# Kernel tuning notes

Measured on AMD Instinct MI355X. Metric: run time of the kernel, lower is better.

Reference implementation:

```python
import math
import jax, jax.numpy as jnp
import numpy as np

QDEPTH = 8
WIDTH = 32
HEIGHT = 32
PIXELS = WIDTH * HEIGHT          # 1024
WIRES = int(math.ceil(math.log2(PIXELS)))  # 10, and PIXELS == 2**WIRES exactly
BATCH = 2048


def setup_inputs() -> dict:
    key = jax.random.key(0)
    k1, k2 = jax.random.split(key)
    x = jax.random.normal(k1, (BATCH, 1, WIDTH, HEIGHT), dtype=jnp.float32)
    # torch.randn(weight_shape) * 0.4
    weights = jax.random.normal(k2, (QDEPTH, WIRES, 3), dtype=jnp.float32) * 0.4
    return {"x": x, "weights": weights, "reps": 1}


def _apply_1q(s, U, wire):
    # s: (batch, 2, 2, ..., 2); apply 2x2 unitary U on qubit `wire` (axis wire+1)
    ax = wire + 1
    s = jnp.moveaxis(s, ax, -1)
    s = s @ U.T                      # new[..., i] = sum_j U[i, j] * old[..., j]
    return jnp.moveaxis(s, -1, ax)


def _apply_cnot(s, ctrl, tgt):
    # flip target bit on the control==1 half of the state
    c_ax = ctrl + 1
    t_ax = tgt + 1
    s0 = jnp.take(s, 0, axis=c_ax)
    s1 = jnp.take(s, 1, axis=c_ax)
    t = t_ax - 1 if t_ax > c_ax else t_ax
    s1 = jnp.flip(s1, axis=t)
    return jnp.stack([s0, s1], axis=c_ax)


def _rot_matrix(phi, theta, omega):
    # qml.Rot = RZ(phi) -> RY(theta) -> RZ(omega)
    c = jnp.cos(theta * 0.5)
    sn = jnp.sin(theta * 0.5)
    ep = jnp.exp(-0.5j * (phi + omega))   # e^{-i(phi+omega)/2}
    em = jnp.exp(-0.5j * (phi - omega))   # e^{-i(phi-omega)/2}
    return jnp.stack([
        jnp.stack([ep * c, -jnp.conj(em) * sn]),
        jnp.stack([em * sn, jnp.conj(ep) * c]),
    ]).astype(jnp.complex64)


def _circuit(psi, weights, reps):
    # psi: (batch, 2**WIRES) complex64 normalized state
    b = psi.shape[0]
    s = psi.reshape((b,) + (2,) * WIRES)
    w = jnp.tanh(weights)                 # qw_map.tanh
    # StronglyEntanglingLayers default ranges: r_l = l % (wires-1) + 1
    ranges = [(l % (WIRES - 1)) + 1 for l in range(QDEPTH)]
    for _ in range(reps):
        for l in range(QDEPTH):
            for q in range(WIRES):
                U = _rot_matrix(w[l, q, 0], w[l, q, 1], w[l, q, 2])
                s = _apply_1q(s, U, q)
            r = ranges[l]
            for q in range(WIRES):
                s = _apply_cnot(s, q, (q + r) % WIRES)
    return s.reshape(b, 2 ** WIRES)


def reference(x, weights, reps):
    b = x.shape[0]
    v = x.reshape(b, PIXELS)                       # b 1 w h -> b (w h)
    old_norm = jnp.linalg.norm(v, axis=-1, keepdims=True)
    psi = (v / old_norm).astype(jnp.complex64)     # real amplitudes, zero imag
    out = _circuit(psi, weights, reps)
    out = out * old_norm.astype(jnp.complex64)
    return out.reshape(b, 1, WIDTH, HEIGHT)
```

## Files before the change

### kernel.cpp

```cpp
#include <hip/hip_runtime.h>
#include <math.h>


#define WIRES   10
#define NSTATE  1024
#define QDEPTH  8
#define NBATCH  2048
#define NGATES  (QDEPTH * WIRES)

typedef float v2f __attribute__((ext_vector_type(2)));
typedef unsigned int v2u __attribute__((ext_vector_type(2)));
static __device__ __forceinline__ v2f s2(float x) { return (v2f){x, x}; }

#define WS_WORDS 1280

__device__ __forceinline__ int perm_g(int j, int r) {
#pragma unroll
    for (int q = WIRES - 1; q >= 0; --q) {
        const int cb = 9 - q;
        const int tb = 9 - ((q + r) % WIRES);
        j ^= ((j >> cb) & 1) << tb;
    }
    return j;
}

__global__ __launch_bounds__(1024) void qprep(
    const float* __restrict__ weights, float* __restrict__ ws)
{
    const int tid = threadIdx.x;
    if (tid < NGATES) {
        const float phi   = tanhf(weights[tid * 3 + 0]);
        const float theta = tanhf(weights[tid * 3 + 1]);
        const float omega = tanhf(weights[tid * 3 + 2]);
        const float c  = cosf(theta * 0.5f);
        const float sn = sinf(theta * 0.5f);
        const float a  = 0.5f * (phi + omega);
        const float bb = 0.5f * (phi - omega);
        const float ca = cosf(a),  sa = sinf(a);
        const float cb = cosf(bb), sb = sinf(bb);
        ws[tid * 8 + 0] =  ca * c;  ws[tid * 8 + 1] = -sa * c;
        ws[tid * 8 + 2] = -cb * sn; ws[tid * 8 + 3] = -sb * sn;
        ws[tid * 8 + 4] =  cb * sn; ws[tid * 8 + 5] = -sb * sn;
        ws[tid * 8 + 6] =  ca * c;  ws[tid * 8 + 7] =  sa * c;
    }
    int* wsI = (int*)ws;
    if (tid >= 128 && tid < 256) {
        const int e = tid - 128, l = e >> 4, t = e & 15;
        const int j = perm_g(t, (l % (WIRES - 1)) + 1);
        wsI[640 + e] = ((j & 15) << 6) | (j >> 4);
    }
    if (tid >= 256 && tid < 768) {
        const int e = tid - 256, l = e >> 6, v = e & 63;
        const int j = perm_g(v << 4, (l % (WIRES - 1)) + 1);
        wsI[768 + e] = ((j & 15) << 6) | (j >> 4);
    }
}

template<int CTRL>
__device__ __forceinline__ float dppmov(float x) {
    return __int_as_float(__builtin_amdgcn_update_dpp(
        0, __float_as_int(x), CTRL, 0xF, 0xF, true));
}
#define FX1(v)  dppmov<0xB1>(v)
#define FX2(v)  dppmov<0x4E>(v)
#define FX4(v)  dppmov<0x1B>(dppmov<0x141>(v))
#define FX8(v)  dppmov<0x128>(v)

#if __has_builtin(__builtin_amdgcn_permlane16_swap)
static __device__ __forceinline__ float pl16swap(float x) {
    const v2u r = __builtin_amdgcn_permlane16_swap(
        __float_as_uint(x), __float_as_uint(x), false, false);
    return __uint_as_float((threadIdx.x & 16) ? r.x : r.y);
}
#define FX16(v) pl16swap(v)
#else
#define FX16(v) __shfl_xor((v), 16, 64)
#endif

#if __has_builtin(__builtin_amdgcn_permlane32_swap)
static __device__ __forceinline__ float pl32swap(float x) {
    const v2u r = __builtin_amdgcn_permlane32_swap(
        __float_as_uint(x), __float_as_uint(x), false, false);
    return __uint_as_float((threadIdx.x & 32) ? r.x : r.y);
}
#define FX32(v) pl32swap(v)
#else
#define FX32(v) __shfl_xor((v), 32, 64)
#endif

#define APPLY_LOCAL_PK(uptr, mask)                                            \
    {                                                                         \
        const float* __restrict__ u = (uptr);                                 \
        const float u00r=u[0], u00i=u[1], u01r=u[2], u01i=u[3];               \
        const float u10r=u[4], u10i=u[5], u11r=u[6], u11i=u[7];               \
        _Pragma("unroll")                                                     \
        for (int k0 = 0; k0 < 8; ++k0) {                                      \
            if (k0 & (mask)) continue;                                        \
            const int k1 = k0 | (mask);                                       \
            const v2f a0r = zr[k0], a0i = zi[k0];                             \
            const v2f a1r = zr[k1], a1i = zi[k1];                             \
            zr[k0] = s2(u00r)*a0r - s2(u00i)*a0i + s2(u01r)*a1r - s2(u01i)*a1i;\
            zi[k0] = s2(u00r)*a0i + s2(u00i)*a0r + s2(u01r)*a1i + s2(u01i)*a1r;\
            zr[k1] = s2(u10r)*a0r - s2(u10i)*a0i + s2(u11r)*a1r - s2(u11i)*a1i;\
            zi[k1] = s2(u10r)*a0i + s2(u10i)*a0r + s2(u11r)*a1i + s2(u11i)*a1r;\
        }                                                                     \
    }

#define LANE_GATE_PK(W, J, FETCH)                                             \
    {                                                                         \
        const float* __restrict__ u = gw + (W) * 8;                           \
        const bool hi = (lane >> (J)) & 1;                                    \
        const float c0r = hi ? u[6] : u[0], c0i = hi ? u[7] : u[1];           \
        const float c1r = hi ? u[4] : u[2], c1i = hi ? u[5] : u[3];           \
        _Pragma("unroll")                                                     \
        for (int k = 0; k < 8; ++k) {                                         \
            v2f pr, pi;                                                       \
            pr.x = FETCH(zr[k].x); pr.y = FETCH(zr[k].y);                     \
            pi.x = FETCH(zi[k].x); pi.y = FETCH(zi[k].y);                     \
            const v2f sr = zr[k], si = zi[k];                                 \
            zr[k] = s2(c0r)*sr - s2(c0i)*si + s2(c1r)*pr - s2(c1i)*pi;        \
            zi[k] = s2(c0r)*si + s2(c0i)*sr + s2(c1r)*pi + s2(c1i)*pr;        \
        }                                                                     \
    }

__global__ __launch_bounds__(64) void qsim_wave(
    const float* __restrict__ x,
    const float* __restrict__ ws,
    float* __restrict__ out,
    const int interleaved)
{
    __shared__ float lds[2 * NSTATE];
    const int lane = threadIdx.x;
    const int b    = blockIdx.x;
    const int* __restrict__ wsI = (const int*)ws;

    v2f zr[8], zi[8];

    const float4* __restrict__ x4 =
        (const float4*)(x + ((size_t)b << 10) + (lane << 4));
    {
        const float4 v0 = x4[0], v1 = x4[1], v2 = x4[2], v3 = x4[3];
        zr[0].x=v0.x; zr[1].x=v0.y; zr[2].x=v0.z; zr[3].x=v0.w;
        zr[4].x=v1.x; zr[5].x=v1.y; zr[6].x=v1.z; zr[7].x=v1.w;
        zr[0].y=v2.x; zr[1].y=v2.y; zr[2].y=v2.z; zr[3].y=v2.w;
        zr[4].y=v3.x; zr[5].y=v3.y; zr[6].y=v3.z; zr[7].y=v3.w;
#pragma unroll
        for (int k = 0; k < 8; ++k) zi[k] = (v2f){0.f, 0.f};
    }

    for (int l = 0; l < QDEPTH; ++l) {
        const float* __restrict__ gw = ws + l * 80;

        APPLY_LOCAL_PK(gw + 9*8, 1)
        APPLY_LOCAL_PK(gw + 8*8, 2)
        APPLY_LOCAL_PK(gw + 7*8, 4)

        {
            const float* __restrict__ u = gw + 6*8;
            const v2f pAr = (v2f){u[0], u[6]};
            const v2f pAi = (v2f){u[1], u[7]};
            const v2f pBr = (v2f){u[2], u[4]};
            const v2f pBi = (v2f){u[3], u[5]};
#pragma unroll
            for (int k = 0; k < 8; ++k) {
                const v2f r  = zr[k], i = zi[k];
                const v2f rs = __builtin_shufflevector(r, r, 1, 0);
                const v2f is = __builtin_shufflevector(i, i, 1, 0);
                zr[k] = pAr*r - pAi*i + pBr*rs - pBi*is;
                zi[k] = pAr*i + pAi*r + pBr*is + pBi*rs;
            }
        }

        LANE_GATE_PK(5, 0, FX1)
        LANE_GATE_PK(4, 1, FX2)
        LANE_GATE_PK(3, 2, FX4)
        LANE_GATE_PK(2, 3, FX8)
        LANE_GATE_PK(1, 4, FX16)
        LANE_GATE_PK(0, 5, FX32)

#pragma unroll
        for (int k = 0; k < 8; ++k) {
            const int w = k * 64 + lane;
            lds[w]        = zr[k].x;
            lds[w + 512]  = zr[k].y;
            lds[w + 1024] = zi[k].x;
            lds[w + 1536] = zi[k].y;
        }
        const int ga = wsI[768 + l * 64 + lane];
#pragma unroll
        for (int k = 0; k < 8; ++k) {
            const int a0 = ga ^ wsI[640 + l * 16 + k];
            const int a1 = ga ^ wsI[640 + l * 16 + k + 8];
            zr[k].x = lds[a0]; zi[k].x = lds[a0 + 1024];
            zr[k].y = lds[a1]; zi[k].y = lds[a1 + 1024];
        }
    }

    if (interleaved) {
        float2* __restrict__ o2 = (float2*)out;
        const size_t base = ((size_t)b << 10) + (lane << 4);
#pragma unroll
        for (int k = 0; k < 8; ++k) {
            o2[base + k]     = make_float2(zr[k].x, zi[k].x);
            o2[base + k + 8] = make_float2(zr[k].y, zi[k].y);
        }
    } else {
        float4* __restrict__ o4 = (float4*)(out + ((size_t)b << 10) + (lane << 4));
        o4[0] = make_float4(zr[0].x, zr[1].x, zr[2].x, zr[3].x);
        o4[1] = make_float4(zr[4].x, zr[5].x, zr[6].x, zr[7].x);
        o4[2] = make_float4(zr[0].y, zr[1].y, zr[2].y, zr[3].y);
        o4[3] = make_float4(zr[4].y, zr[5].y, zr[6].y, zr[7].y);
    }
}

__global__ __launch_bounds__(256) void qcircuit_kernel(
    const float* __restrict__ x, const float* __restrict__ weights,
    float* __restrict__ out, const int interleaved)
{
    __shared__ float s_re[NSTATE];
    __shared__ float s_im[NSTATE];
    __shared__ float s_g[NGATES][8];
    const int tid = threadIdx.x;
    const int b   = blockIdx.x;
    if (tid < NGATES) {
        const float phi   = tanhf(weights[tid * 3 + 0]);
        const float theta = tanhf(weights[tid * 3 + 1]);
        const float omega = tanhf(weights[tid * 3 + 2]);
        const float c  = cosf(theta * 0.5f);
        const float sn = sinf(theta * 0.5f);
        const float a  = 0.5f * (phi + omega);
        const float bb = 0.5f * (phi - omega);
        const float ca = cosf(a),  sa = sinf(a);
        const float cb = cosf(bb), sb = sinf(bb);
        s_g[tid][0] =  ca * c;  s_g[tid][1] = -sa * c;
        s_g[tid][2] = -cb * sn; s_g[tid][3] = -sb * sn;
        s_g[tid][4] =  cb * sn; s_g[tid][5] = -sb * sn;
        s_g[tid][6] =  ca * c;  s_g[tid][7] =  sa * c;
    }
#pragma unroll
    for (int k = 0; k < 4; ++k) {
        const int i = tid + 256 * k;
        s_re[i] = x[b * NSTATE + i];
        s_im[i] = 0.0f;
    }
    __syncthreads();
    for (int l = 0; l < QDEPTH; ++l) {
        for (int q = 0; q < WIRES; ++q) {
            const int gi = l * WIRES + q;
            const float u00r = s_g[gi][0], u00i = s_g[gi][1];
            const float u01r = s_g[gi][2], u01i = s_g[gi][3];
            const float u10r = s_g[gi][4], u10i = s_g[gi][5];
            const float u11r = s_g[gi][6], u11i = s_g[gi][7];
            const int sh = 9 - q;
            const int m  = 1 << sh;
#pragma unroll
            for (int k = 0; k < 2; ++k) {
                const int p  = tid + 256 * k;
                const int i0 = ((p >> sh) << (sh + 1)) | (p & (m - 1));
                const int i1 = i0 | m;
                const float a0r = s_re[i0], a0i = s_im[i0];
                const float a1r = s_re[i1], a1i = s_im[i1];
                s_re[i0] = u00r*a0r - u00i*a0i + u01r*a1r - u01i*a1i;
                s_im[i0] = u00r*a0i + u00i*a0r + u01r*a1i + u01i*a1r;
                s_re[i1] = u10r*a0r - u10i*a0i + u11r*a1r - u11i*a1i;
                s_im[i1] = u10r*a0i + u10i*a0r + u11r*a1i + u11i*a1r;
            }
            __syncthreads();
        }
        const int r = (l % (WIRES - 1)) + 1;
        float vr[4], vi[4];
#pragma unroll
        for (int k = 0; k < 4; ++k) {
            const int i = tid + 256 * k;
            const int j = perm_g(i, r);
            vr[k] = s_re[j]; vi[k] = s_im[j];
        }
        __syncthreads();
#pragma unroll
        for (int k = 0; k < 4; ++k) {
            const int i = tid + 256 * k;
            s_re[i] = vr[k]; s_im[i] = vi[k];
        }
        __syncthreads();
    }
    if (interleaved) {
#pragma unroll
        for (int k = 0; k < 4; ++k) {
            const int i  = tid + 256 * k;
            const int fi = 2 * (b * NSTATE + i);
            out[fi + 0] = s_re[i];
            out[fi + 1] = s_im[i];
        }
    } else {
#pragma unroll
        for (int k = 0; k < 4; ++k) {
            const int i = tid + 256 * k;
            out[b * NSTATE + i] = s_re[i];
        }
    }
}

extern "C" void kernel_launch(void* const* d_in, const int* in_sizes, int n_in,
                              void* d_out, int out_size, void* d_ws, size_t ws_size,
                              hipStream_t stream) {
    const float* x       = (const float*)d_in[0];
    const float* weights = (const float*)d_in[1];
    float* out = (float*)d_out;
    const int interleaved = (out_size >= 2 * NBATCH * NSTATE) ? 1 : 0;

    if (ws_size >= WS_WORDS * sizeof(float)) {
        float* ws = (float*)d_ws;
        qprep<<<1, 1024, 0, stream>>>(weights, ws);
        qsim_wave<<<NBATCH, 64, 0, stream>>>(x, ws, out, interleaved);
    } else {
        qcircuit_kernel<<<NBATCH, 256, 0, stream>>>(x, weights, out, interleaved);
    }
}
```

Measured before the change: 104.4 us.

## Split each batch state across two wavefronts with LDS exchange for one qubit

Each batch element's 1024-amplitude state is now spread over two 64-lane wavefronts instead of one, so each thread holds 4 packed register pairs rather than 8. One qubit that used to be local to a thread now spans the two waves, and its gate is applied by exchanging amplitudes through a shared-memory buffer behind a barrier. The goal is shorter per-thread dependency chains, lower register pressure and more waves in flight. The cost is two block-level barriers per layer and extra LDS traffic.

```diff
diff --git a/kernel.cpp b/kernel.cpp
--- a/kernel.cpp
+++ b/kernel.cpp
@@ -88,15 +88,15 @@
 #define FX32(v) __shfl_xor((v), 32, 64)
 #endif
 
-#define APPLY_LOCAL_PK(uptr, mask)                                            \
+#define APPLY_LOCAL_PK4(uptr, mask)                                           \
     {                                                                         \
         const float* __restrict__ u = (uptr);                                 \
         const float u00r=u[0], u00i=u[1], u01r=u[2], u01i=u[3];               \
         const float u10r=u[4], u10i=u[5], u11r=u[6], u11i=u[7];               \
         _Pragma("unroll")                                                     \
-        for (int k0 = 0; k0 < 8; ++k0) {                                      \
+        for (int k0 = 0; k0 < 4; ++k0) {                                      \
             if (k0 & (mask)) continue;                                        \
-            const int k1 = k0 | (mask);                                       \
+            const int k1 = k0 | (mask);                                      \
             const v2f a0r = zr[k0], a0i = zi[k0];                             \
             const v2f a1r = zr[k1], a1i = zi[k1];                             \
             zr[k0] = s2(u00r)*a0r - s2(u00i)*a0i + s2(u01r)*a1r - s2(u01i)*a1i;\
@@ -106,14 +106,14 @@
         }                                                                     \
     }
 
-#define LANE_GATE_PK(W, J, FETCH)                                             \
+#define LANE_GATE_PK4(W, J, FETCH)                                            \
     {                                                                         \
         const float* __restrict__ u = gw + (W) * 8;                           \
         const bool hi = (lane >> (J)) & 1;                                    \
         const float c0r = hi ? u[6] : u[0], c0i = hi ? u[7] : u[1];           \
         const float c1r = hi ? u[4] : u[2], c1i = hi ? u[5] : u[3];           \
         _Pragma("unroll")                                                     \
-        for (int k = 0; k < 8; ++k) {                                         \
+        for (int k = 0; k < 4; ++k) {                                         \
             v2f pr, pi;                                                       \
             pr.x = FETCH(zr[k].x); pr.y = FETCH(zr[k].y);                     \
             pi.x = FETCH(zi[k].x); pi.y = FETCH(zi[k].y);                     \
@@ -123,46 +123,47 @@
         }                                                                     \
     }
 
-__global__ __launch_bounds__(64) void qsim_wave(
+__global__ __launch_bounds__(128) void qsim_wave2(
     const float* __restrict__ x,
     const float* __restrict__ ws,
     float* __restrict__ out,
     const int interleaved)
 {
     __shared__ float lds[2 * NSTATE];
-    const int lane = threadIdx.x;
+    __shared__ v2f exb[2 * 4 * 2 * 64];
+
+    const int tid  = threadIdx.x;
+    const int lane = tid & 63;
+    const int w    = tid >> 6;
     const int b    = blockIdx.x;
     const int* __restrict__ wsI = (const int*)ws;
 
-    v2f zr[8], zi[8];
+    v2f zr[4], zi[4];
 
     const float4* __restrict__ x4 =
-        (const float4*)(x + ((size_t)b << 10) + (lane << 4));
+        (const float4*)(x + ((size_t)b << 10) + (lane << 4) + (w << 3));
     {
-        const float4 v0 = x4[0], v1 = x4[1], v2 = x4[2], v3 = x4[3];
+        const float4 v0 = x4[0], v1 = x4[1];
         zr[0].x=v0.x; zr[1].x=v0.y; zr[2].x=v0.z; zr[3].x=v0.w;
-        zr[4].x=v1.x; zr[5].x=v1.y; zr[6].x=v1.z; zr[7].x=v1.w;
-        zr[0].y=v2.x; zr[1].y=v2.y; zr[2].y=v2.z; zr[3].y=v2.w;
-        zr[4].y=v3.x; zr[5].y=v3.y; zr[6].y=v3.z; zr[7].y=v3.w;
-#pragma unroll
-        for (int k = 0; k < 8; ++k) zi[k] = (v2f){0.f, 0.f};
+        zr[0].y=v1.x; zr[1].y=v1.y; zr[2].y=v1.z; zr[3].y=v1.w;
+#pragma unroll
+        for (int k = 0; k < 4; ++k) zi[k] = (v2f){0.f, 0.f};
     }
 
     for (int l = 0; l < QDEPTH; ++l) {
         const float* __restrict__ gw = ws + l * 80;
 
-        APPLY_LOCAL_PK(gw + 9*8, 1)
-        APPLY_LOCAL_PK(gw + 8*8, 2)
-        APPLY_LOCAL_PK(gw + 7*8, 4)
+        APPLY_LOCAL_PK4(gw + 9*8, 1)
+        APPLY_LOCAL_PK4(gw + 8*8, 2)
 
         {
-            const float* __restrict__ u = gw + 6*8;
+            const float* __restrict__ u = gw + 7*8;
             const v2f pAr = (v2f){u[0], u[6]};
             const v2f pAi = (v2f){u[1], u[7]};
             const v2f pBr = (v2f){u[2], u[4]};
             const v2f pBi = (v2f){u[3], u[5]};
 #pragma unroll
-            for (int k = 0; k < 8; ++k) {
+            for (int k = 0; k < 4; ++k) {
                 const v2f r  = zr[k], i = zi[k];
                 const v2f rs = __builtin_shufflevector(r, r, 1, 0);
                 const v2f is = __builtin_shufflevector(i, i, 1, 0);
@@ -171,26 +172,49 @@
             }
         }
 
-        LANE_GATE_PK(5, 0, FX1)
-        LANE_GATE_PK(4, 1, FX2)
-        LANE_GATE_PK(3, 2, FX4)
-        LANE_GATE_PK(2, 3, FX8)
-        LANE_GATE_PK(1, 4, FX16)
-        LANE_GATE_PK(0, 5, FX32)
-
-#pragma unroll
-        for (int k = 0; k < 8; ++k) {
-            const int w = k * 64 + lane;
-            lds[w]        = zr[k].x;
-            lds[w + 512]  = zr[k].y;
-            lds[w + 1024] = zi[k].x;
-            lds[w + 1536] = zi[k].y;
-        }
+        {
+            const int wb = w * 512 + lane;
+            exb[wb +   0] = zr[0]; exb[wb +  64] = zi[0];
+            exb[wb + 128] = zr[1]; exb[wb + 192] = zi[1];
+            exb[wb + 256] = zr[2]; exb[wb + 320] = zi[2];
+            exb[wb + 384] = zr[3]; exb[wb + 448] = zi[3];
+            __syncthreads();
+            const float* __restrict__ u = gw + 6*8;
+            const bool hi = (w != 0);
+            const float c0r = hi ? u[6] : u[0], c0i = hi ? u[7] : u[1];
+            const float c1r = hi ? u[4] : u[2], c1i = hi ? u[5] : u[3];
+            const int pb = (w ^ 1) * 512 + lane;
+#pragma unroll
+            for (int k = 0; k < 4; ++k) {
+                const v2f pr = exb[pb + k * 128];
+                const v2f pi = exb[pb + k * 128 + 64];
+                const v2f sr = zr[k], si = zi[k];
+                zr[k] = s2(c0r)*sr - s2(c0i)*si + s2(c1r)*pr - s2(c1i)*pi;
+                zi[k] = s2(c0r)*si + s2(c0i)*sr + s2(c1r)*pi + s2(c1i)*pr;
+            }
+        }
+
+        LANE_GATE_PK4(5, 0, FX1)
+        LANE_GATE_PK4(4, 1, FX2)
+        LANE_GATE_PK4(3, 2, FX4)
+        LANE_GATE_PK4(2, 3, FX8)
+        LANE_GATE_PK4(1, 4, FX16)
+        LANE_GATE_PK4(0, 5, FX32)
+
+#pragma unroll
+        for (int k = 0; k < 4; ++k) {
+            const int ww = (w * 8 + k) * 64 + lane;
+            lds[ww]        = zr[k].x;
+            lds[ww + 256]  = zr[k].y;
+            lds[ww + 1024] = zi[k].x;
+            lds[ww + 1280] = zi[k].y;
+        }
+        __syncthreads();
         const int ga = wsI[768 + l * 64 + lane];
 #pragma unroll
-        for (int k = 0; k < 8; ++k) {
-            const int a0 = ga ^ wsI[640 + l * 16 + k];
-            const int a1 = ga ^ wsI[640 + l * 16 + k + 8];
+        for (int k = 0; k < 4; ++k) {
+            const int a0 = ga ^ wsI[640 + l * 16 + w * 8 + k];
+            const int a1 = ga ^ wsI[640 + l * 16 + w * 8 + k + 4];
             zr[k].x = lds[a0]; zi[k].x = lds[a0 + 1024];
             zr[k].y = lds[a1]; zi[k].y = lds[a1 + 1024];
         }
@@ -198,18 +222,17 @@
 
     if (interleaved) {
         float2* __restrict__ o2 = (float2*)out;
-        const size_t base = ((size_t)b << 10) + (lane << 4);
-#pragma unroll
-        for (int k = 0; k < 8; ++k) {
+        const size_t base = ((size_t)b << 10) + (lane << 4) + (w << 3);
+#pragma unroll
+        for (int k = 0; k < 4; ++k) {
             o2[base + k]     = make_float2(zr[k].x, zi[k].x);
-            o2[base + k + 8] = make_float2(zr[k].y, zi[k].y);
+            o2[base + k + 4] = make_float2(zr[k].y, zi[k].y);
         }
     } else {
-        float4* __restrict__ o4 = (float4*)(out + ((size_t)b << 10) + (lane << 4));
+        float4* __restrict__ o4 =
+            (float4*)(out + ((size_t)b << 10) + (lane << 4) + (w << 3));
         o4[0] = make_float4(zr[0].x, zr[1].x, zr[2].x, zr[3].x);
-        o4[1] = make_float4(zr[4].x, zr[5].x, zr[6].x, zr[7].x);
-        o4[2] = make_float4(zr[0].y, zr[1].y, zr[2].y, zr[3].y);
-        o4[3] = make_float4(zr[4].y, zr[5].y, zr[6].y, zr[7].y);
+        o4[1] = make_float4(zr[0].y, zr[1].y, zr[2].y, zr[3].y);
     }
 }
 
@@ -311,7 +334,7 @@
     if (ws_size >= WS_WORDS * sizeof(float)) {
         float* ws = (float*)d_ws;
         qprep<<<1, 1024, 0, stream>>>(weights, ws);
-        qsim_wave<<<NBATCH, 64, 0, stream>>>(x, ws, out, interleaved);
+        qsim_wave2<<<NBATCH, 128, 0, stream>>>(x, ws, out, interleaved);
     } else {
         qcircuit_kernel<<<NBATCH, 256, 0, stream>>>(x, weights, out, interleaved);
     }
```

Result: slower. 109.2 us (+4.6%).

## Process two batch states per wavefront to interleave independent gate chains

Applied to the files above, without the earlier changes.

Each 64-lane block now simulates two batch samples at once, holding two register-resident states and interleaving their gate applications, lane shuffles and LDS CNOT permutations. The grid is halved to 1024 blocks and LDS per block doubles. The aim is more instruction-level parallelism to hide shuffle and LDS latency, and amortised gate-weight loads. The cost is doubled register pressure, which may lower occupancy, and fewer blocks to spread across the CUs.

```diff
diff --git a/kernel.cpp b/kernel.cpp
--- a/kernel.cpp
+++ b/kernel.cpp
@@ -88,7 +88,7 @@
 #define FX32(v) __shfl_xor((v), 32, 64)
 #endif
 
-#define APPLY_LOCAL_PK(uptr, mask)                                            \
+#define APPLY_LOCAL_PK(uptr, mask, zr, zi)                                    \
     {                                                                         \
         const float* __restrict__ u = (uptr);                                 \
         const float u00r=u[0], u00i=u[1], u01r=u[2], u01i=u[3];               \
@@ -106,7 +106,24 @@
         }                                                                     \
     }
 
-#define LANE_GATE_PK(W, J, FETCH)                                             \
+#define HALF_SWAP_PK(uptr, zr, zi)                                            \
+    {                                                                         \
+        const float* __restrict__ u = (uptr);                                 \
+        const v2f pAr = (v2f){u[0], u[6]};                  \
+        const v2f pAi = (v2f){u[1], u[7]};                  \
+        const v2f pBr = (v2f){u[2], u[4]};                  \
+        const v2f pBi = (v2f){u[3], u[5]};                  \
+        _Pragma("unroll")                                                     \
+        for (int k = 0; k < 8; ++k) {                                         \
+            const v2f r  = zr[k], i = zi[k];                                  \
+            const v2f rs = __builtin_shufflevector(r, r, 1, 0);               \
+            const v2f is = __builtin_shufflevector(i, i, 1, 0);               \
+            zr[k] = pAr*r - pAi*i + pBr*rs - pBi*is;                          \
+            zi[k] = pAr*i + pAi*r + pBr*is + pBi*rs;                          \
+        }                                                                     \
+    }
+
+#define LANE_GATE_PK(W, J, FETCH, zr, zi)                                     \
     {                                                                         \
         const float* __restrict__ u = gw + (W) * 8;                           \
         const bool hi = (lane >> (J)) & 1;                                    \
@@ -123,93 +140,113 @@
         }                                                                     \
     }
 
-__global__ __launch_bounds__(64) void qsim_wave(
+#define CNOT_WRITE(zr, zi, BASE)                                              \
+    _Pragma("unroll")                                                         \
+    for (int k = 0; k < 8; ++k) {                                             \
+        const int w = (BASE) + k * 64 + lane;                                 \
+        lds[w]        = zr[k].x;                                              \
+        lds[w + 512]  = zr[k].y;                                              \
+        lds[w + 1024] = zi[k].x;                                              \
+        lds[w + 1536] = zi[k].y;                                              \
+    }
+
+#define CNOT_READ(zr, zi, BASE)                                               \
+    _Pragma("unroll")                                                         \
+    for (int k = 0; k < 8; ++k) {                                             \
+        const int a0 = ga ^ wsI[640 + l * 16 + k];                            \
+        const int a1 = ga ^ wsI[640 + l * 16 + k + 8];                        \
+        zr[k].x = lds[(BASE) + a0]; zi[k].x = lds[(BASE) + a0 + 1024];        \
+        zr[k].y = lds[(BASE) + a1]; zi[k].y = lds[(BASE) + a1 + 1024];        \
+    }
+
+#define LOAD_STATE(x4, zr, zi)                                                \
+    {                                                                         \
+        const float4 v0 = (x4)[0], v1 = (x4)[1], v2 = (x4)[2], v3 = (x4)[3];  \
+        zr[0].x=v0.x; zr[1].x=v0.y; zr[2].x=v0.z; zr[3].x=v0.w;               \
+        zr[4].x=v1.x; zr[5].x=v1.y; zr[6].x=v1.z; zr[7].x=v1.w;               \
+        zr[0].y=v2.x; zr[1].y=v2.y; zr[2].y=v2.z; zr[3].y=v2.w;               \
+        zr[4].y=v3.x; zr[5].y=v3.y; zr[6].y=v3.z; zr[7].y=v3.w;               \
+        _Pragma("unroll")                                                     \
+        for (int k = 0; k < 8; ++k) zi[k] = (v2f){0.f, 0.f};                  \
+    }
+
+__global__ __launch_bounds__(64) void qsim_dual(
     const float* __restrict__ x,
     const float* __restrict__ ws,
     float* __restrict__ out,
     const int interleaved)
 {
-    __shared__ float lds[2 * NSTATE];
+    __shared__ float lds[4 * NSTATE];
     const int lane = threadIdx.x;
     const int b    = blockIdx.x;
     const int* __restrict__ wsI = (const int*)ws;
 
-    v2f zr[8], zi[8];
-
-    const float4* __restrict__ x4 =
-        (const float4*)(x + ((size_t)b << 10) + (lane << 4));
-    {
-        const float4 v0 = x4[0], v1 = x4[1], v2 = x4[2], v3 = x4[3];
-        zr[0].x=v0.x; zr[1].x=v0.y; zr[2].x=v0.z; zr[3].x=v0.w;
-        zr[4].x=v1.x; zr[5].x=v1.y; zr[6].x=v1.z; zr[7].x=v1.w;
-        zr[0].y=v2.x; zr[1].y=v2.y; zr[2].y=v2.z; zr[3].y=v2.w;
-        zr[4].y=v3.x; zr[5].y=v3.y; zr[6].y=v3.z; zr[7].y=v3.w;
-#pragma unroll
-        for (int k = 0; k < 8; ++k) zi[k] = (v2f){0.f, 0.f};
-    }
+    v2f zrA[8], ziA[8], zrB[8], ziB[8];
+
+    const float4* __restrict__ x4A =
+        (const float4*)(x + ((size_t)(2 * b) << 10) + (lane << 4));
+    const float4* __restrict__ x4B =
+        (const float4*)(x + ((size_t)(2 * b + 1) << 10) + (lane << 4));
+    LOAD_STATE(x4A, zrA, ziA)
+    LOAD_STATE(x4B, zrB, ziB)
 
     for (int l = 0; l < QDEPTH; ++l) {
         const float* __restrict__ gw = ws + l * 80;
 
-        APPLY_LOCAL_PK(gw + 9*8, 1)
-        APPLY_LOCAL_PK(gw + 8*8, 2)
-        APPLY_LOCAL_PK(gw + 7*8, 4)
-
-        {
-            const float* __restrict__ u = gw + 6*8;
-            const v2f pAr = (v2f){u[0], u[6]};
-            const v2f pAi = (v2f){u[1], u[7]};
-            const v2f pBr = (v2f){u[2], u[4]};
-            const v2f pBi = (v2f){u[3], u[5]};
-#pragma unroll
-            for (int k = 0; k < 8; ++k) {
-                const v2f r  = zr[k], i = zi[k];
-                const v2f rs = __builtin_shufflevector(r, r, 1, 0);
-                const v2f is = __builtin_shufflevector(i, i, 1, 0);
-                zr[k] = pAr*r - pAi*i + pBr*rs - pBi*is;
-                zi[k] = pAr*i + pAi*r + pBr*is + pBi*rs;
-            }
-        }
-
-        LANE_GATE_PK(5, 0, FX1)
-        LANE_GATE_PK(4, 1, FX2)
-        LANE_GATE_PK(3, 2, FX4)
-        LANE_GATE_PK(2, 3, FX8)
-        LANE_GATE_PK(1, 4, FX16)
-        LANE_GATE_PK(0, 5, FX32)
-
-#pragma unroll
-        for (int k = 0; k < 8; ++k) {
-            const int w = k * 64 + lane;
-            lds[w]        = zr[k].x;
-            lds[w + 512]  = zr[k].y;
-            lds[w + 1024] = zi[k].x;
-            lds[w + 1536] = zi[k].y;
-        }
+        APPLY_LOCAL_PK(gw + 9*8, 1, zrA, ziA)
+        APPLY_LOCAL_PK(gw + 9*8, 1, zrB, ziB)
+        APPLY_LOCAL_PK(gw + 8*8, 2, zrA, ziA)
+        APPLY_LOCAL_PK(gw + 8*8, 2, zrB, ziB)
+        APPLY_LOCAL_PK(gw + 7*8, 4, zrA, ziA)
+        APPLY_LOCAL_PK(gw + 7*8, 4, zrB, ziB)
+
+        HALF_SWAP_PK(gw + 6*8, zrA, ziA)
+        HALF_SWAP_PK(gw + 6*8, zrB, ziB)
+
+        LANE_GATE_PK(5, 0, FX1,  zrA, ziA)
+        LANE_GATE_PK(5, 0, FX1,  zrB, ziB)
+        LANE_GATE_PK(4, 1, FX2,  zrA, ziA)
+        LANE_GATE_PK(4, 1, FX2,  zrB, ziB)
+        LANE_GATE_PK(3, 2, FX4,  zrA, ziA)
+        LANE_GATE_PK(3, 2, FX4,  zrB, ziB)
+        LANE_GATE_PK(2, 3, FX8,  zrA, ziA)
+        LANE_GATE_PK(2, 3, FX8,  zrB, ziB)
+        LANE_GATE_PK(1, 4, FX16, zrA, ziA)
+        LANE_GATE_PK(1, 4, FX16, zrB, ziB)
+        LANE_GATE_PK(0, 5, FX32, zrA, ziA)
+        LANE_GATE_PK(0, 5, FX32, zrB, ziB)
+
+        CNOT_WRITE(zrA, ziA, 0)
+        CNOT_WRITE(zrB, ziB, 2048)
         const int ga = wsI[768 + l * 64 + lane];
-#pragma unroll
-        for (int k = 0; k < 8; ++k) {
-            const int a0 = ga ^ wsI[640 + l * 16 + k];
-            const int a1 = ga ^ wsI[640 + l * 16 + k + 8];
-            zr[k].x = lds[a0]; zi[k].x = lds[a0 + 1024];
-            zr[k].y = lds[a1]; zi[k].y = lds[a1 + 1024];
-        }
+        CNOT_READ(zrA, ziA, 0)
+        CNOT_READ(zrB, ziB, 2048)
     }
 
     if (interleaved) {
         float2* __restrict__ o2 = (float2*)out;
-        const size_t base = ((size_t)b << 10) + (lane << 4);
+        const size_t baseA = ((size_t)(2 * b) << 10) + (lane << 4);
+        const size_t baseB = ((size_t)(2 * b + 1) << 10) + (lane << 4);
 #pragma unroll
         for (int k = 0; k < 8; ++k) {
-            o2[base + k]     = make_float2(zr[k].x, zi[k].x);
-            o2[base + k + 8] = make_float2(zr[k].y, zi[k].y);
+            o2[baseA + k]     = make_float2(zrA[k].x, ziA[k].x);
+            o2[baseA + k + 8] = make_float2(zrA[k].y, ziA[k].y);
+            o2[baseB + k]     = make_float2(zrB[k].x, ziB[k].x);
+            o2[baseB + k + 8] = make_float2(zrB[k].y, ziB[k].y);
         }
     } else {
-        float4* __restrict__ o4 = (float4*)(out + ((size_t)b << 10) + (lane << 4));
-        o4[0] = make_float4(zr[0].x, zr[1].x, zr[2].x, zr[3].x);
-        o4[1] = make_float4(zr[4].x, zr[5].x, zr[6].x, zr[7].x);
-        o4[2] = make_float4(zr[0].y, zr[1].y, zr[2].y, zr[3].y);
-        o4[3] = make_float4(zr[4].y, zr[5].y, zr[6].y, zr[7].y);
+        float4* __restrict__ o4A =
+            (float4*)(out + ((size_t)(2 * b) << 10) + (lane << 4));
+        float4* __restrict__ o4B =
+            (float4*)(out + ((size_t)(2 * b + 1) << 10) + (lane << 4));
+        o4A[0] = make_float4(zrA[0].x, zrA[1].x, zrA[2].x, zrA[3].x);
+        o4A[1] = make_float4(zrA[4].x, zrA[5].x, zrA[6].x, zrA[7].x);
+        o4A[2] = make_float4(zrA[0].y, zrA[1].y, zrA[2].y, zrA[3].y);
+        o4A[3] = make_float4(zrA[4].y, zrA[5].y, zrA[6].y, zrA[7].y);
+        o4B[0] = make_float4(zrB[0].x, zrB[1].x, zrB[2].x, zrB[3].x);
+        o4B[1] = make_float4(zrB[4].x, zrB[5].x, zrB[6].x, zrB[7].x);
+        o4B[2] = make_float4(zrB[0].y, zrB[1].y, zrB[2].y, zrB[3].y);
+        o4B[3] = make_float4(zrB[4].y, zrB[5].y, zrB[6].y, zrB[7].y);
     }
 }
 
@@ -311,7 +348,7 @@
     if (ws_size >= WS_WORDS * sizeof(float)) {
         float* ws = (float*)d_ws;
         qprep<<<1, 1024, 0, stream>>>(weights, ws);
-        qsim_wave<<<NBATCH, 64, 0, stream>>>(x, ws, out, interleaved);
+        qsim_dual<<<NBATCH / 2, 64, 0, stream>>>(x, ws, out, interleaved);
     } else {
         qcircuit_kernel<<<NBATCH, 256, 0, stream>>>(x, weights, out, interleaved);
     }
```

Measured after the change: 124.6 us. +19.4%, slower.
